# Kernel optimization log

Measured on AMD Instinct MI355X. Metric: run time of the kernel, lower is better.

The kernel has to match this reference:

```python
import jax, jax.numpy as jnp
import numpy as np

D_MODEL = 2048
NUM_HEADS = 16
D_K = D_MODEL // NUM_HEADS  # 128, per-head dim used for RoPE
ROPE_THETA = 10000.0
MAX_SEQ_LEN = 2048
BATCH = 4
SEQ = 2048


def _trunc_normal(key, shape, std):
    # approximate trunc_normal_(mean=0, std, a=-3std, b=3std)
    return jnp.clip(std * jax.random.normal(key, shape), -3 * std, 3 * std)


def setup_inputs() -> dict:
    key = jax.random.key(0)
    ks = jax.random.split(key, 6)
    x = jax.random.normal(ks[0], (BATCH, SEQ, D_MODEL), dtype=jnp.float32)
    token_positions = jnp.arange(SEQ, dtype=jnp.int32)
    std = float(np.sqrt(2.0 / (D_MODEL + D_MODEL)))
    wq = _trunc_normal(ks[1], (D_MODEL, D_MODEL), std)  # (d_out, d_in)
    wk = _trunc_normal(ks[2], (D_MODEL, D_MODEL), std)
    wv = _trunc_normal(ks[3], (D_MODEL, D_MODEL), std)
    wo = _trunc_normal(ks[4], (D_MODEL, D_MODEL), std)
    return {"x": x, "token_positions": token_positions,
            "wq": wq, "wk": wk, "wv": wv, "wo": wo}


def _rope(t, pos):
    # t: (b, h, n, d_k), pos: (n,) int
    # interleaved pairs: (x1, x2) = (t[..., 0::2], t[..., 1::2])
    freqs = 1.0 / (ROPE_THETA ** (jnp.arange(0, D_K, 2, dtype=jnp.float32) / D_K))
    angles = pos.astype(jnp.float32)[:, None] * freqs[None, :]  # (n, d_k/2)
    cos = jnp.cos(angles).astype(t.dtype)
    sin = jnp.sin(angles).astype(t.dtype)
    tr = t.reshape(*t.shape[:-1], D_K // 2, 2)
    x1, x2 = tr[..., 0], tr[..., 1]
    y1 = cos * x1 - sin * x2
    y2 = sin * x1 + cos * x2
    return jnp.stack([y1, y2], axis=-1).reshape(t.shape)


def reference(x, token_positions, wq, wk, wv, wo):
    b, n, d = x.shape
    q = jnp.einsum('bnd,od->bno', x, wq)
    k = jnp.einsum('bnd,od->bno', x, wk)
    v = jnp.einsum('bnd,od->bno', x, wv)
    # split heads for RoPE: (b, n, h*dk) -> (b, h, n, dk)
    split = lambda t: t.reshape(b, n, NUM_HEADS, D_K).transpose(0, 2, 1, 3)
    merge = lambda t: t.transpose(0, 2, 1, 3).reshape(b, n, d)
    q = merge(_rope(split(q), token_positions))
    k = merge(_rope(split(k), token_positions))
    # NOTE: source merges heads back BEFORE flash attention -> single-head
    # attention over full d_model with causal mask, scale 1/sqrt(d_model)
    scale = 1.0 / jnp.sqrt(jnp.asarray(d, dtype=x.dtype))
    scores = jnp.einsum('bqd,bkd->bqk', q, k) * scale  # (b, n, n)
    causal = jnp.tril(jnp.ones((n, n), dtype=bool))
    scores = jnp.where(causal[None, :, :], scores, jnp.finfo(scores.dtype).min)
    attn = jax.nn.softmax(scores, axis=-1)
    out = jnp.einsum('bqk,bkd->bqd', attn, v)
    return jnp.einsum('bnd,od->bno', out, wo)
```

## Files before the change

### kernel.cpp

```cpp
#include <hip/hip_runtime.h>
#include <hip/hip_bf16.h>
#include <cstdint>
#include <cmath>

typedef __attribute__((ext_vector_type(4))) float f32x4;
typedef __attribute__((ext_vector_type(8))) short bf16x8;

#define BAR()   __builtin_amdgcn_s_barrier()
#define PRIO1() __builtin_amdgcn_s_setprio(1)
#define PRIO0() __builtin_amdgcn_s_setprio(0)
#define WAITV6() asm volatile("s_waitcnt vmcnt(6)" ::: "memory")
#define WAITV4() asm volatile("s_waitcnt vmcnt(4)" ::: "memory")
#define WAITV0() asm volatile("s_waitcnt vmcnt(0)" ::: "memory")
#define MM(a,b,c) __builtin_amdgcn_mfma_f32_16x16x32_bf16((a),(b),(c),0,0,0)

__device__ __forceinline__ void gl_lds16(const __hip_bfloat16* g, char* l) {
    __builtin_amdgcn_global_load_lds(
        (const __attribute__((address_space(1))) void*)g,
        (__attribute__((address_space(3))) void*)l, 16, 0, 0);
}
__device__ __forceinline__ void store_c(float* C, size_t i, float v) { C[i] = v; }
__device__ __forceinline__ void store_c(__hip_bfloat16* C, size_t i, float v) { C[i] = __float2bfloat16(v); }

#define SGA8(dd, h, i, kt) do{ const int s_ = (h)*16 + (i)*8 + w; \
    gl_lds16(Asb + (size_t)((s_>>1)<<4) * lda + ((s_&1)<<5) + (kt), \
             lds + (dd)*65536 + (s_<<10)); }while(0)
#define SGB8N(dd, g, kt) do{ const int sB_ = (g)*8 + w; \
    const int hi_ = sB_ >> 4, r_ = sB_ & 15; \
    const int wc_ = r_ >> 2, ni_ = hi_*2 + ((r_>>1)&1), kk_ = r_ & 1; \
    gl_lds16(Bsb + (size_t)(wc_*64 + ni_*16) * ldb + (kk_<<5) + (kt), \
             lds + (dd)*65536 + 32768 + (sB_<<10)); }while(0)
#define LDA8(dd, miA, kk) (*(const bf16x8*)(lds + (dd)*65536 + ((sbA + (miA)*2 + (kk)) << 10) + rswz))
#define LDB8N(dd, ni, kk) (*(const bf16x8*)(lds + (dd)*65536 + 32768 + \
    ((((((ni)>>1)<<4) + ((w&3)<<2) + (((ni)&1)<<1) + (kk))) << 10) + rswz))

template<typename CT>
__global__ __launch_bounds__(512, 2)
void gemm8p(const __hip_bfloat16* __restrict__ A, const __hip_bfloat16* __restrict__ B,
            CT* __restrict__ C, int K, int lda, int ldb, int ldc, int nbx, float alpha)
{
    __shared__ __align__(1024) char lds[131072];

    const int nwg = gridDim.x;
    const int q8 = nwg >> 3, r8 = nwg & 7;
    const int xcd = blockIdx.x & 7, blk = blockIdx.x >> 3;
    const int wg = (xcd < r8 ? xcd * (q8 + 1) : r8 * (q8 + 1) + (xcd - r8) * q8) + blk;
    const int bm0 = (wg / nbx) * 256, bn0 = (wg % nbx) * 256;

    const int tid  = threadIdx.x;
    const int lane = tid & 63;
    const int w    = tid >> 6;

    const int rb   = (lane & 15) * 64 + (lane >> 4) * 16;
    const int rswz = rb ^ (((rb >> 9) & 1) << 5);
    const int sbA  = (w >> 2) * 16;

    const int l16 = lane * 16;
    const int uqs = l16 ^ (((l16 >> 9) & 1) << 5);
    const int rIn = uqs >> 6;
    const int cIn = (uqs & 63) >> 1;
    const __hip_bfloat16* Asb = A + (size_t)(bm0 + rIn) * lda + cIn;
    const __hip_bfloat16* Bsb = B + (size_t)(bn0 + rIn) * ldb + cIn;

    f32x4 acc[8][4] = {};
    bf16x8 afA[4][2], bfB[2][2];

    const int nt = K >> 6;

    SGA8(0, 0, 0, 0); SGA8(0, 1, 0, 0);
    SGB8N(0, 0, 0);   SGB8N(0, 1, 0);
    SGB8N(0, 2, 0);   SGB8N(0, 3, 0);
    SGA8(0, 0, 1, 0); SGA8(0, 1, 1, 0);
    if (nt > 1) {
        SGA8(1, 0, 0, 64); SGA8(1, 1, 0, 64);
        SGB8N(1, 2, 64);   SGB8N(1, 3, 64);
        SGA8(1, 0, 1, 64); SGA8(1, 1, 1, 64);
        WAITV6();
    } else WAITV0();
    BAR();

    for (int t = 0; t < nt; ++t) {
        const int d   = t & 1, e = d ^ 1;
        const bool p1 = (t + 1) < nt;
        const bool p2 = (t + 2) < nt;
        const int kt1 = (t + 1) << 6;
        const int kt2 = (t + 2) << 6;

#pragma unroll
        for (int mi = 0; mi < 4; ++mi) { afA[mi][0] = LDA8(d, mi, 0); afA[mi][1] = LDA8(d, mi, 1); }
#pragma unroll
        for (int ni = 0; ni < 2; ++ni) { bfB[ni][0] = LDB8N(d, ni, 0); bfB[ni][1] = LDB8N(d, ni, 1); }
        if (p1) { SGB8N(e, 0, kt1); SGB8N(e, 1, kt1); }
        BAR();
        PRIO1();
#pragma unroll
        for (int mi = 0; mi < 4; ++mi)
#pragma unroll
            for (int ni = 0; ni < 2; ++ni) {
                f32x4 c = acc[mi][ni];
                c = MM(afA[mi][0], bfB[ni][0], c);
                c = MM(afA[mi][1], bfB[ni][1], c);
                acc[mi][ni] = c;
            }
        PRIO0();
        BAR();

#pragma unroll
        for (int ni = 0; ni < 2; ++ni) { bfB[ni][0] = LDB8N(d, 2 + ni, 0); bfB[ni][1] = LDB8N(d, 2 + ni, 1); }
        if (p2) { SGA8(d, 0, 0, kt2); SGA8(d, 1, 0, kt2); }
        BAR();
        PRIO1();
#pragma unroll
        for (int mi = 0; mi < 4; ++mi)
#pragma unroll
            for (int ni = 0; ni < 2; ++ni) {
                f32x4 c = acc[mi][2 + ni];
                c = MM(afA[mi][0], bfB[ni][0], c);
                c = MM(afA[mi][1], bfB[ni][1], c);
                acc[mi][2 + ni] = c;
            }
        PRIO0();
        BAR();

#pragma unroll
        for (int mi = 0; mi < 4; ++mi) { afA[mi][0] = LDA8(d, 4 + mi, 0); afA[mi][1] = LDA8(d, 4 + mi, 1); }
        if (p2) { SGB8N(d, 2, kt2); SGB8N(d, 3, kt2); }
        BAR();
        PRIO1();
#pragma unroll
        for (int mi = 0; mi < 4; ++mi)
#pragma unroll
            for (int ni = 0; ni < 2; ++ni) {
                f32x4 c = acc[4 + mi][2 + ni];
                c = MM(afA[mi][0], bfB[ni][0], c);
                c = MM(afA[mi][1], bfB[ni][1], c);
                acc[4 + mi][2 + ni] = c;
            }
        PRIO0();
        BAR();

#pragma unroll
        for (int ni = 0; ni < 2; ++ni) { bfB[ni][0] = LDB8N(d, ni, 0); bfB[ni][1] = LDB8N(d, ni, 1); }
        if (p2) { SGA8(d, 0, 1, kt2); SGA8(d, 1, 1, kt2); WAITV6(); }
        else WAITV0();
        BAR();
        PRIO1();
#pragma unroll
        for (int mi = 0; mi < 4; ++mi)
#pragma unroll
            for (int ni = 0; ni < 2; ++ni) {
                f32x4 c = acc[4 + mi][ni];
                c = MM(afA[mi][0], bfB[ni][0], c);
                c = MM(afA[mi][1], bfB[ni][1], c);
                acc[4 + mi][ni] = c;
            }
        PRIO0();
        BAR();
    }

    const int cr = (lane >> 4) * 4, cc = lane & 15;
    const int wrow = bm0 + (w >> 2) * 128, wcol = bn0 + (w & 3) * 64;
#pragma unroll
    for (int mi = 0; mi < 8; ++mi)
#pragma unroll
        for (int ni = 0; ni < 4; ++ni) {
            const int row = wrow + mi * 16 + cr;
            const int col = wcol + ni * 16 + cc;
#pragma unroll
            for (int j = 0; j < 4; ++j)
                store_c(C, (size_t)(row + j) * ldc + col, acc[mi][ni][j] * alpha);
        }
}

#define STAGEA(nb, kt) do{ gl_lds16(Asrc + (kt),                        lds + (nb)         + wb); \
                           gl_lds16(Asrc + (size_t)128 * lda + (kt),    lds + (nb) +  8192 + wb);}while(0)
#define STAGEB(nb, kt) do{ gl_lds16(Bsrc + (kt),                        lds + (nb) + 16384 + wb); \
                           gl_lds16(Bsrc + (size_t)128 * ldb + (kt),    lds + (nb) + 24576 + wb);}while(0)

template<typename CT, int MODE>
__global__ __launch_bounds__(512, 2)
void gemm256(const __hip_bfloat16* __restrict__ A, const __hip_bfloat16* __restrict__ B,
             CT* __restrict__ C, int K, int lda, int ldb, int ldc, int nbx,
             float alpha, size_t sA, size_t sB, size_t sC)
{
    __shared__ __align__(1024) char lds[98304];

    int bm0, bn0;
    if (MODE == 1) {
        const int wgi = blockIdx.x;
        int by = (int)((sqrtf(8.f * wgi + 1.f) - 1.f) * 0.5f);
        if (by * (by + 1) / 2 > wgi) --by;
        if ((by + 1) * (by + 2) / 2 <= wgi) ++by;
        const int bx = wgi - by * (by + 1) / 2;
        bm0 = by * 256; bn0 = bx * 256;
    } else if (MODE == 2) {
        const int g = blockIdx.x;
        const int nby = gridDim.x / nbx;
        const int bx = g % nbx;
        const int by = (g / nbx + bx) % nby;
        bm0 = by * 256; bn0 = bx * 256;
    } else {
        const int nwg = gridDim.x;
        const int q8 = nwg >> 3, r8 = nwg & 7;
        const int xcd = blockIdx.x & 7, blk = blockIdx.x >> 3;
        const int wg = (xcd < r8 ? xcd * (q8 + 1) : r8 * (q8 + 1) + (xcd - r8) * q8) + blk;
        bm0 = (wg / nbx) * 256; bn0 = (wg % nbx) * 256;
    }

    A += sA * blockIdx.y; B += sB * blockIdx.y; C += sC * blockIdx.y;

    const int tid  = threadIdx.x;
    const int lane = tid & 63;
    const int w    = tid >> 6;
    const int wb   = w * 1024;

    const int rb   = (lane & 15) * 64 + (lane >> 4) * 16;
    const int rswz = rb ^ (((rb >> 9) & 1) << 5);
    const int srA  = (w >> 2) * 8;
    const int srB  = (w & 3) * 4;

    const int q0 = tid * 16;
    const int uq = q0 ^ (((q0 >> 9) & 1) << 5);
    const int r0 = ((q0 >> 10) << 4) | ((uq >> 6) & 15);
    const int c0 = (uq & 63) >> 1;
    const __hip_bfloat16* Asrc = A + (size_t)(bm0 + r0) * lda + c0;
    const __hip_bfloat16* Bsrc = B + (size_t)(bn0 + r0) * ldb + c0;

    f32x4 acc[8][4] = {};
    bf16x8 af[4], bf[4];

    const int klim = bm0 + 256;
    const int kend = (MODE == 2) ? (K < klim ? K : klim) : K;
    const int nt   = kend >> 5;

    STAGEA(0, 0); STAGEB(0, 0);
    if (nt > 1) { STAGEA(32768, 32); STAGEB(32768, 32); }

    for (int t = 0; t < nt; ++t) {
        if (t + 1 < nt) WAITV4(); else WAITV0();
        BAR();
        const char* dA = lds + (t % 3) * 32768;
        const char* dB = dA + 16384;
        const int  nbo = ((t + 2) % 3) * 32768;
        const bool pf  = (t + 2 < nt);
        const int  kt  = (t + 2) << 5;

#pragma unroll
        for (int i = 0; i < 4; ++i) af[i] = *(const bf16x8*)(dA + ((srA + i) << 10) + rswz);
#pragma unroll
        for (int i = 0; i < 4; ++i) bf[i] = *(const bf16x8*)(dB + ((srB + i) << 10) + rswz);
        if (pf) STAGEA(nbo, kt);
        BAR();
        PRIO1();
#pragma unroll
        for (int mi = 0; mi < 4; ++mi)
#pragma unroll
            for (int ni = 0; ni < 4; ++ni)
                acc[mi][ni] = MM(af[mi], bf[ni], acc[mi][ni]);
        PRIO0();

#pragma unroll
        for (int i = 0; i < 4; ++i) af[i] = *(const bf16x8*)(dA + ((srA + 4 + i) << 10) + rswz);
        if (pf) STAGEB(nbo, kt);
        BAR();
        PRIO1();
#pragma unroll
        for (int mi = 0; mi < 4; ++mi)
#pragma unroll
            for (int ni = 0; ni < 4; ++ni)
                acc[4 + mi][ni] = MM(af[mi], bf[ni], acc[4 + mi][ni]);
        PRIO0();
    }

    const int cr = (lane >> 4) * 4, cc = lane & 15;
    const int wrow = bm0 + (w >> 2) * 128, wcol = bn0 + (w & 3) * 64;
#pragma unroll
    for (int mi = 0; mi < 8; ++mi)
#pragma unroll
        for (int ni = 0; ni < 4; ++ni) {
            const int row = wrow + mi * 16 + cr;
            const int col = wcol + ni * 16 + cc;
#pragma unroll
            for (int j = 0; j < 4; ++j)
                store_c(C, (size_t)(row + j) * ldc + col, acc[mi][ni][j] * alpha);
        }
}

__global__ void f32_to_bf16_vec(const float* __restrict__ in,
                                __hip_bfloat16* __restrict__ out, int n4)
{
    int i = blockIdx.x * 256 + threadIdx.x;
    if (i >= n4) return;
    float4 v = ((const float4*)in)[i];
    union { ushort4 u; __hip_bfloat16 h[4]; } o;
    o.h[0] = __float2bfloat16(v.x);
    o.h[1] = __float2bfloat16(v.y);
    o.h[2] = __float2bfloat16(v.z);
    o.h[3] = __float2bfloat16(v.w);
    ((ushort4*)out)[i] = o.u;
}

__global__ void conv_w4(const float* __restrict__ w0, const float* __restrict__ w1,
                        const float* __restrict__ w2, const float* __restrict__ w3,
                        __hip_bfloat16* o0, __hip_bfloat16* o1,
                        __hip_bfloat16* o2, __hip_bfloat16* o3, int n4)
{
    int i = blockIdx.x * 256 + threadIdx.x;
    if (i >= n4) return;
    const float* src; __hip_bfloat16* dst;
    switch (blockIdx.y) {
        case 0: src = w0; dst = o0; break;
        case 1: src = w1; dst = o1; break;
        case 2: src = w2; dst = o2; break;
        default: src = w3; dst = o3; break;
    }
    float4 v = ((const float4*)src)[i];
    union { ushort4 u; __hip_bfloat16 h[4]; } o;
    o.h[0] = __float2bfloat16(v.x);
    o.h[1] = __float2bfloat16(v.y);
    o.h[2] = __float2bfloat16(v.z);
    o.h[3] = __float2bfloat16(v.w);
    ((ushort4*)dst)[i] = o.u;
}

__global__ void rope_table(const int* __restrict__ pos, float2* __restrict__ tab, int N)
{
    int i = blockIdx.x * 256 + threadIdx.x;
    if (i >= N * 64) return;
    int n = i >> 6, j = i & 63;
    float p = (float)pos[n];
    float ang = p * powf(10000.f, -(float)j * (1.0f / 64.0f));
    tab[i] = make_float2(cosf(ang), sinf(ang));
}

__global__ void rope_apply2(__hip_bfloat16* __restrict__ Q, __hip_bfloat16* __restrict__ K,
                            const float2* __restrict__ tab, int ld)
{
    int i = blockIdx.x * 256 + threadIdx.x;
    __hip_bfloat16* T = blockIdx.y ? K : Q;
    int r  = i >> 8;
    int cb = (i & 255) << 3;
    int n  = r & 2047;
    int j0 = (cb >> 1) & 63;
    union { bf16x8 v; __hip_bfloat162 h[4]; } u;
    __hip_bfloat16* p = T + (size_t)r * ld + cb;
    u.v = *(const bf16x8*)p;
#pragma unroll
    for (int k = 0; k < 4; ++k) {
        float2 cs = tab[(n << 6) + j0 + k];
        float x1 = __bfloat162float(u.h[k].x);
        float x2 = __bfloat162float(u.h[k].y);
        u.h[k].x = __float2bfloat16(cs.x * x1 - cs.y * x2);
        u.h[k].y = __float2bfloat16(cs.y * x1 + cs.x * x2);
    }
    *(bf16x8*)p = u.v;
}

__global__ void softmax_causal_ip(float* __restrict__ S, int N)
{
    const int q = blockIdx.x;
    float* srow = S + ((size_t)blockIdx.y * N + q) * N;
    __shared__ float buf[2048];
    __shared__ float red[8];
    const int tid = threadIdx.x;
    const int wend = ((q >> 8) + 1) << 8;

    float4* b4 = (float4*)buf;
    const float4* s4 = (const float4*)srow;
    for (int i = tid; i <= (q >> 2); i += 256) b4[i] = s4[i];
    __syncthreads();

    float m = -1e30f;
    for (int j = tid; j <= q; j += 256) m = fmaxf(m, buf[j]);
#pragma unroll
    for (int o = 32; o > 0; o >>= 1) m = fmaxf(m, __shfl_xor(m, o));
    if ((tid & 63) == 0) red[tid >> 6] = m;
    __syncthreads();
    m = fmaxf(fmaxf(red[0], red[1]), fmaxf(red[2], red[3]));

    float sum = 0.f;
    for (int j = tid; j <= q; j += 256) { float e = __expf(buf[j] - m); buf[j] = e; sum += e; }
#pragma unroll
    for (int o = 32; o > 0; o >>= 1) sum += __shfl_xor(sum, o);
    if ((tid & 63) == 0) red[4 + (tid >> 6)] = sum;
    __syncthreads();
    const float inv = 1.f / (red[4] + red[5] + red[6] + red[7]);

    __hip_bfloat162* p2 = (__hip_bfloat162*)srow;
    for (int i = tid; i < (wend >> 1); i += 256) {
        int j0 = i * 2;
        __hip_bfloat162 h;
        h.x = __float2bfloat16(j0     <= q ? buf[j0]     * inv : 0.f);
        h.y = __float2bfloat16(j0 + 1 <= q ? buf[j0 + 1] * inv : 0.f);
        p2[i] = h;
    }
}

__global__ void transpose_bf16(const __hip_bfloat16* __restrict__ V,
                               __hip_bfloat16* __restrict__ Vt, int N, int ldv)
{
    __shared__ __hip_bfloat16 tile[32][33];
    const size_t bi = (size_t)blockIdx.z * N * ldv;
    const size_t bo = (size_t)blockIdx.z * N * N;
    const int k0 = blockIdx.x * 32, d0 = blockIdx.y * 32;
    const int tx = threadIdx.x, ty = threadIdx.y;
#pragma unroll
    for (int j = 0; j < 4; ++j)
        tile[ty + 8 * j][tx] = V[bi + (size_t)(k0 + ty + 8 * j) * ldv + d0 + tx];
    __syncthreads();
#pragma unroll
    for (int j = 0; j < 4; ++j)
        Vt[bo + (size_t)(d0 + ty + 8 * j) * N + k0 + tx] = tile[tx][ty + 8 * j];
}

extern "C" void kernel_launch(void* const* d_in, const int* in_sizes, int n_in,
                              void* d_out, int out_size, void* d_ws, size_t ws_size,
                              hipStream_t stream)
{
    const float* x  = (const float*)d_in[0];
    const int* pos  = (const int*)d_in[1];
    const float* wq = (const float*)d_in[2];
    const float* wk = (const float*)d_in[3];
    const float* wv = (const float*)d_in[4];
    const float* wo = (const float*)d_in[5];
    float* out = (float*)d_out;

    const int B = 4, N = 2048, D = 2048;
    const int M = B * N;
    const int D3 = 3 * D;
    const size_t MB = 1ull << 20;
    if (ws_size < 192 * MB) return;

    char* w = (char*)d_ws;
    __hip_bfloat16* QKV  = (__hip_bfloat16*)(w + 0 * MB);
    __hip_bfloat16* wqkv = (__hip_bfloat16*)(w + 96 * MB);
    __hip_bfloat16* wob  = (__hip_bfloat16*)(w + 120 * MB);
    __hip_bfloat16* xb   = (__hip_bfloat16*)(w + 128 * MB);
    __hip_bfloat16* Vt   = xb;
    __hip_bfloat16* AO   = (__hip_bfloat16*)(w + 160 * MB);
    float2*         tab  = (float2*)(w + 190 * MB);

    __hip_bfloat16* Qb = QKV;
    __hip_bfloat16* Kb = QKV + D;
    __hip_bfloat16* Vb = QKV + 2 * D;

    float* Sal = (float*)d_out;

    f32_to_bf16_vec<<<(M * D / 4 + 255) / 256, 256, 0, stream>>>(x, xb, M * D / 4);
    conv_w4<<<dim3((D * D / 4 + 255) / 256, 4), 256, 0, stream>>>(
        wq, wk, wv, wo, wqkv, wqkv + (size_t)D * D, wqkv + (size_t)2 * D * D, wob, D * D / 4);
    rope_table<<<(N * 64 + 255) / 256, 256, 0, stream>>>(pos, tab, N);

    gemm8p<__hip_bfloat16><<<dim3((D3 / 256) * (M / 256)), 512, 0, stream>>>(
        xb, wqkv, QKV, D, D, D, D3, D3 / 256, 1.f);

    rope_apply2<<<dim3(M, 2), 256, 0, stream>>>(Qb, Kb, tab, D3);

    transpose_bf16<<<dim3(N / 32, N / 32, B), dim3(32, 8), 0, stream>>>(Vb, Vt, N, D3);

    const float scale = 1.0f / sqrtf((float)D);
    const int nbxA = N / 256;
    const int ntri = nbxA * (nbxA + 1) / 2;
    gemm256<float, 1><<<dim3(ntri, B), 512, 0, stream>>>(
        Qb, Kb, Sal, D, D3, D3, N, nbxA, scale,
        (size_t)N * D3, (size_t)N * D3, (size_t)N * N);
    softmax_causal_ip<<<dim3(N, B), 256, 0, stream>>>(Sal, N);
    gemm256<__hip_bfloat16, 2><<<dim3(nbxA * nbxA, B), 512, 0, stream>>>(
        (const __hip_bfloat16*)Sal, Vt, AO, N, 2 * N, N, D, nbxA, 1.f,
        (size_t)2 * N * N, (size_t)N * N, (size_t)N * D);

    gemm256<float, 0><<<dim3((D / 256) * (M / 256)), 512, 0, stream>>>(
        AO, wob, out, D, D, D, D, D / 256, 1.f, 0, 0, 0);
}
```

Before: 463.1 us.

## Unify GEMMs into one 64-wide-K kernel with register-prefetched LDS fragments

Merges the two GEMM kernels into a single templated gemm8p that carries gemm256's MODE-based block mapping (triangular, causal-limited K, plain). The K tile grows from 32 to 64. The loop uses double-buffered register fragments (afA0/afA1, bfB0/bfB1) so the LDS reads for the next phase are issued during the current MFMA block instead of before it, which is meant to hide LDS latency behind matrix math. This raises LDS use to 128KB and increases register pressure, and the QK^T, PV and output-projection GEMMs now all go through this schedule.

```diff
diff --git a/kernel.cpp b/kernel.cpp
--- a/kernel.cpp
+++ b/kernel.cpp
@@ -9,8 +9,8 @@
 #define BAR()   __builtin_amdgcn_s_barrier()
 #define PRIO1() __builtin_amdgcn_s_setprio(1)
 #define PRIO0() __builtin_amdgcn_s_setprio(0)
+#define WAITV8() asm volatile("s_waitcnt vmcnt(8)" ::: "memory")
 #define WAITV6() asm volatile("s_waitcnt vmcnt(6)" ::: "memory")
-#define WAITV4() asm volatile("s_waitcnt vmcnt(4)" ::: "memory")
 #define WAITV0() asm volatile("s_waitcnt vmcnt(0)" ::: "memory")
 #define MM(a,b,c) __builtin_amdgcn_mfma_f32_16x16x32_bf16((a),(b),(c),0,0,0)
 
@@ -34,156 +34,13 @@
 #define LDB8N(dd, ni, kk) (*(const bf16x8*)(lds + (dd)*65536 + 32768 + \
     ((((((ni)>>1)<<4) + ((w&3)<<2) + (((ni)&1)<<1) + (kk))) << 10) + rswz))
 
-template<typename CT>
+template<typename CT, int MODE>
 __global__ __launch_bounds__(512, 2)
 void gemm8p(const __hip_bfloat16* __restrict__ A, const __hip_bfloat16* __restrict__ B,
-            CT* __restrict__ C, int K, int lda, int ldb, int ldc, int nbx, float alpha)
+            CT* __restrict__ C, int K, int lda, int ldb, int ldc, int nbx,
+            float alpha, size_t sA, size_t sB, size_t sC)
 {
     __shared__ __align__(1024) char lds[131072];
-
-    const int nwg = gridDim.x;
-    const int q8 = nwg >> 3, r8 = nwg & 7;
-    const int xcd = blockIdx.x & 7, blk = blockIdx.x >> 3;
-    const int wg = (xcd < r8 ? xcd * (q8 + 1) : r8 * (q8 + 1) + (xcd - r8) * q8) + blk;
-    const int bm0 = (wg / nbx) * 256, bn0 = (wg % nbx) * 256;
-
-    const int tid  = threadIdx.x;
-    const int lane = tid & 63;
-    const int w    = tid >> 6;
-
-    const int rb   = (lane & 15) * 64 + (lane >> 4) * 16;
-    const int rswz = rb ^ (((rb >> 9) & 1) << 5);
-    const int sbA  = (w >> 2) * 16;
-
-    const int l16 = lane * 16;
-    const int uqs = l16 ^ (((l16 >> 9) & 1) << 5);
-    const int rIn = uqs >> 6;
-    const int cIn = (uqs & 63) >> 1;
-    const __hip_bfloat16* Asb = A + (size_t)(bm0 + rIn) * lda + cIn;
-    const __hip_bfloat16* Bsb = B + (size_t)(bn0 + rIn) * ldb + cIn;
-
-    f32x4 acc[8][4] = {};
-    bf16x8 afA[4][2], bfB[2][2];
-
-    const int nt = K >> 6;
-
-    SGA8(0, 0, 0, 0); SGA8(0, 1, 0, 0);
-    SGB8N(0, 0, 0);   SGB8N(0, 1, 0);
-    SGB8N(0, 2, 0);   SGB8N(0, 3, 0);
-    SGA8(0, 0, 1, 0); SGA8(0, 1, 1, 0);
-    if (nt > 1) {
-        SGA8(1, 0, 0, 64); SGA8(1, 1, 0, 64);
-        SGB8N(1, 2, 64);   SGB8N(1, 3, 64);
-        SGA8(1, 0, 1, 64); SGA8(1, 1, 1, 64);
-        WAITV6();
-    } else WAITV0();
-    BAR();
-
-    for (int t = 0; t < nt; ++t) {
-        const int d   = t & 1, e = d ^ 1;
-        const bool p1 = (t + 1) < nt;
-        const bool p2 = (t + 2) < nt;
-        const int kt1 = (t + 1) << 6;
-        const int kt2 = (t + 2) << 6;
-
-#pragma unroll
-        for (int mi = 0; mi < 4; ++mi) { afA[mi][0] = LDA8(d, mi, 0); afA[mi][1] = LDA8(d, mi, 1); }
-#pragma unroll
-        for (int ni = 0; ni < 2; ++ni) { bfB[ni][0] = LDB8N(d, ni, 0); bfB[ni][1] = LDB8N(d, ni, 1); }
-        if (p1) { SGB8N(e, 0, kt1); SGB8N(e, 1, kt1); }
-        BAR();
-        PRIO1();
-#pragma unroll
-        for (int mi = 0; mi < 4; ++mi)
-#pragma unroll
-            for (int ni = 0; ni < 2; ++ni) {
-                f32x4 c = acc[mi][ni];
-                c = MM(afA[mi][0], bfB[ni][0], c);
-                c = MM(afA[mi][1], bfB[ni][1], c);
-                acc[mi][ni] = c;
-            }
-        PRIO0();
-        BAR();
-
-#pragma unroll
-        for (int ni = 0; ni < 2; ++ni) { bfB[ni][0] = LDB8N(d, 2 + ni, 0); bfB[ni][1] = LDB8N(d, 2 + ni, 1); }
-        if (p2) { SGA8(d, 0, 0, kt2); SGA8(d, 1, 0, kt2); }
-        BAR();
-        PRIO1();
-#pragma unroll
-        for (int mi = 0; mi < 4; ++mi)
-#pragma unroll
-            for (int ni = 0; ni < 2; ++ni) {
-                f32x4 c = acc[mi][2 + ni];
-                c = MM(afA[mi][0], bfB[ni][0], c);
-                c = MM(afA[mi][1], bfB[ni][1], c);
-                acc[mi][2 + ni] = c;
-            }
-        PRIO0();
-        BAR();
-
-#pragma unroll
-        for (int mi = 0; mi < 4; ++mi) { afA[mi][0] = LDA8(d, 4 + mi, 0); afA[mi][1] = LDA8(d, 4 + mi, 1); }
-        if (p2) { SGB8N(d, 2, kt2); SGB8N(d, 3, kt2); }
-        BAR();
-        PRIO1();
-#pragma unroll
-        for (int mi = 0; mi < 4; ++mi)
-#pragma unroll
-            for (int ni = 0; ni < 2; ++ni) {
-                f32x4 c = acc[4 + mi][2 + ni];
-                c = MM(afA[mi][0], bfB[ni][0], c);
-                c = MM(afA[mi][1], bfB[ni][1], c);
-                acc[4 + mi][2 + ni] = c;
-            }
-        PRIO0();
-        BAR();
-
-#pragma unroll
-        for (int ni = 0; ni < 2; ++ni) { bfB[ni][0] = LDB8N(d, ni, 0); bfB[ni][1] = LDB8N(d, ni, 1); }
-        if (p2) { SGA8(d, 0, 1, kt2); SGA8(d, 1, 1, kt2); WAITV6(); }
-        else WAITV0();
-        BAR();
-        PRIO1();
-#pragma unroll
-        for (int mi = 0; mi < 4; ++mi)
-#pragma unroll
-            for (int ni = 0; ni < 2; ++ni) {
-                f32x4 c = acc[4 + mi][ni];
-                c = MM(afA[mi][0], bfB[ni][0], c);
-                c = MM(afA[mi][1], bfB[ni][1], c);
-                acc[4 + mi][ni] = c;
-            }
-        PRIO0();
-        BAR();
-    }
-
-    const int cr = (lane >> 4) * 4, cc = lane & 15;
-    const int wrow = bm0 + (w >> 2) * 128, wcol = bn0 + (w & 3) * 64;
-#pragma unroll
-    for (int mi = 0; mi < 8; ++mi)
-#pragma unroll
-        for (int ni = 0; ni < 4; ++ni) {
-            const int row = wrow + mi * 16 + cr;
-            const int col = wcol + ni * 16 + cc;
-#pragma unroll
-            for (int j = 0; j < 4; ++j)
-                store_c(C, (size_t)(row + j) * ldc + col, acc[mi][ni][j] * alpha);
-        }
-}
-
-#define STAGEA(nb, kt) do{ gl_lds16(Asrc + (kt),                        lds + (nb)         + wb); \
-                           gl_lds16(Asrc + (size_t)128 * lda + (kt),    lds + (nb) +  8192 + wb);}while(0)
-#define STAGEB(nb, kt) do{ gl_lds16(Bsrc + (kt),                        lds + (nb) + 16384 + wb); \
-                           gl_lds16(Bsrc + (size_t)128 * ldb + (kt),    lds + (nb) + 24576 + wb);}while(0)
-
-template<typename CT, int MODE>
-__global__ __launch_bounds__(512, 2)
-void gemm256(const __hip_bfloat16* __restrict__ A, const __hip_bfloat16* __restrict__ B,
-             CT* __restrict__ C, int K, int lda, int ldb, int ldc, int nbx,
-             float alpha, size_t sA, size_t sB, size_t sC)
-{
-    __shared__ __align__(1024) char lds[98304];
 
     int bm0, bn0;
     if (MODE == 1) {
@@ -212,64 +69,122 @@
     const int tid  = threadIdx.x;
     const int lane = tid & 63;
     const int w    = tid >> 6;
-    const int wb   = w * 1024;
 
     const int rb   = (lane & 15) * 64 + (lane >> 4) * 16;
     const int rswz = rb ^ (((rb >> 9) & 1) << 5);
-    const int srA  = (w >> 2) * 8;
-    const int srB  = (w & 3) * 4;
-
-    const int q0 = tid * 16;
-    const int uq = q0 ^ (((q0 >> 9) & 1) << 5);
-    const int r0 = ((q0 >> 10) << 4) | ((uq >> 6) & 15);
-    const int c0 = (uq & 63) >> 1;
-    const __hip_bfloat16* Asrc = A + (size_t)(bm0 + r0) * lda + c0;
-    const __hip_bfloat16* Bsrc = B + (size_t)(bn0 + r0) * ldb + c0;
+    const int sbA  = (w >> 2) * 16;
+
+    const int l16 = lane * 16;
+    const int uqs = l16 ^ (((l16 >> 9) & 1) << 5);
+    const int rIn = uqs >> 6;
+    const int cIn = (uqs & 63) >> 1;
+    const __hip_bfloat16* Asb = A + (size_t)(bm0 + rIn) * lda + cIn;
+    const __hip_bfloat16* Bsb = B + (size_t)(bn0 + rIn) * ldb + cIn;
 
     f32x4 acc[8][4] = {};
-    bf16x8 af[4], bf[4];
+    bf16x8 afA0[4][2], afA1[4][2], bfB0[2][2], bfB1[2][2];
 
     const int klim = bm0 + 256;
     const int kend = (MODE == 2) ? (K < klim ? K : klim) : K;
-    const int nt   = kend >> 5;
-
-    STAGEA(0, 0); STAGEB(0, 0);
-    if (nt > 1) { STAGEA(32768, 32); STAGEB(32768, 32); }
+    const int nt   = kend >> 6;
+
+    SGA8(0, 0, 0, 0); SGA8(0, 1, 0, 0);
+    SGB8N(0, 0, 0);   SGB8N(0, 1, 0);
+    SGB8N(0, 2, 0);   SGB8N(0, 3, 0);
+    SGA8(0, 0, 1, 0); SGA8(0, 1, 1, 0);
+    if (nt > 1) {
+        SGA8(1, 0, 0, 64); SGA8(1, 1, 0, 64);
+        SGB8N(1, 2, 64);   SGB8N(1, 3, 64);
+        SGA8(1, 0, 1, 64); SGA8(1, 1, 1, 64);
+        WAITV6();
+    } else WAITV0();
+    BAR();
+#pragma unroll
+    for (int mi = 0; mi < 4; ++mi) { afA0[mi][0] = LDA8(0, mi, 0); afA0[mi][1] = LDA8(0, mi, 1); }
+#pragma unroll
+    for (int ni = 0; ni < 2; ++ni) { bfB0[ni][0] = LDB8N(0, ni, 0); bfB0[ni][1] = LDB8N(0, ni, 1); }
 
     for (int t = 0; t < nt; ++t) {
-        if (t + 1 < nt) WAITV4(); else WAITV0();
-        BAR();
-        const char* dA = lds + (t % 3) * 32768;
-        const char* dB = dA + 16384;
-        const int  nbo = ((t + 2) % 3) * 32768;
-        const bool pf  = (t + 2 < nt);
-        const int  kt  = (t + 2) << 5;
-
-#pragma unroll
-        for (int i = 0; i < 4; ++i) af[i] = *(const bf16x8*)(dA + ((srA + i) << 10) + rswz);
-#pragma unroll
-        for (int i = 0; i < 4; ++i) bf[i] = *(const bf16x8*)(dB + ((srB + i) << 10) + rswz);
-        if (pf) STAGEA(nbo, kt);
+        const int d   = t & 1, e = d ^ 1;
+        const bool p1 = (t + 1) < nt;
+        const bool p2 = (t + 2) < nt;
+        const int kt1 = (t + 1) << 6;
+        const int kt2 = (t + 2) << 6;
+
+        if (p1) { SGB8N(e, 0, kt1); SGB8N(e, 1, kt1); }
         BAR();
         PRIO1();
 #pragma unroll
         for (int mi = 0; mi < 4; ++mi)
 #pragma unroll
-            for (int ni = 0; ni < 4; ++ni)
-                acc[mi][ni] = MM(af[mi], bf[ni], acc[mi][ni]);
+            for (int ni = 0; ni < 2; ++ni) {
+                f32x4 c = acc[mi][ni];
+                c = MM(afA0[mi][0], bfB0[ni][0], c);
+                c = MM(afA0[mi][1], bfB0[ni][1], c);
+                acc[mi][ni] = c;
+            }
+#pragma unroll
+        for (int ni = 0; ni < 2; ++ni) { bfB1[ni][0] = LDB8N(d, 2 + ni, 0); bfB1[ni][1] = LDB8N(d, 2 + ni, 1); }
         PRIO0();
-
-#pragma unroll
-        for (int i = 0; i < 4; ++i) af[i] = *(const bf16x8*)(dA + ((srA + 4 + i) << 10) + rswz);
-        if (pf) STAGEB(nbo, kt);
+        BAR();
+
+        if (p2) { SGA8(d, 0, 0, kt2); SGA8(d, 1, 0, kt2); WAITV8(); }
+        else if (p1) WAITV6();
+        else WAITV0();
         BAR();
         PRIO1();
 #pragma unroll
         for (int mi = 0; mi < 4; ++mi)
 #pragma unroll
-            for (int ni = 0; ni < 4; ++ni)
-                acc[4 + mi][ni] = MM(af[mi], bf[ni], acc[4 + mi][ni]);
+            for (int ni = 0; ni < 2; ++ni) {
+                f32x4 c = acc[mi][2 + ni];
+                c = MM(afA0[mi][0], bfB1[ni][0], c);
+                c = MM(afA0[mi][1], bfB1[ni][1], c);
+                acc[mi][2 + ni] = c;
+            }
+#pragma unroll
+        for (int mi = 0; mi < 4; ++mi) { afA1[mi][0] = LDA8(d, 4 + mi, 0); afA1[mi][1] = LDA8(d, 4 + mi, 1); }
         PRIO0();
+        BAR();
+
+        if (p2) { SGB8N(d, 2, kt2); SGB8N(d, 3, kt2); }
+        BAR();
+        PRIO1();
+#pragma unroll
+        for (int mi = 0; mi < 4; ++mi)
+#pragma unroll
+            for (int ni = 0; ni < 2; ++ni) {
+                f32x4 c = acc[4 + mi][2 + ni];
+                c = MM(afA1[mi][0], bfB1[ni][0], c);
+                c = MM(afA1[mi][1], bfB1[ni][1], c);
+                acc[4 + mi][2 + ni] = c;
+            }
+        if (p1) {
+#pragma unroll
+            for (int mi = 0; mi < 4; ++mi) { afA0[mi][0] = LDA8(e, mi, 0); afA0[mi][1] = LDA8(e, mi, 1); }
+        }
+        PRIO0();
+        BAR();
+
+        if (p2) { SGA8(d, 0, 1, kt2); SGA8(d, 1, 1, kt2); WAITV6(); }
+        else WAITV0();
+        BAR();
+        PRIO1();
+#pragma unroll
+        for (int mi = 0; mi < 4; ++mi)
+#pragma unroll
+            for (int ni = 0; ni < 2; ++ni) {
+                f32x4 c = acc[4 + mi][ni];
+                c = MM(afA1[mi][0], bfB0[ni][0], c);
+                c = MM(afA1[mi][1], bfB0[ni][1], c);
+                acc[4 + mi][ni] = c;
+            }
+        if (p1) {
+#pragma unroll
+            for (int ni = 0; ni < 2; ++ni) { bfB0[ni][0] = LDB8N(e, ni, 0); bfB0[ni][1] = LDB8N(e, ni, 1); }
+        }
+        PRIO0();
+        BAR();
     }
 
     const int cr = (lane >> 4) * 4, cc = lane & 15;
@@ -451,8 +366,8 @@
         wq, wk, wv, wo, wqkv, wqkv + (size_t)D * D, wqkv + (size_t)2 * D * D, wob, D * D / 4);
     rope_table<<<(N * 64 + 255) / 256, 256, 0, stream>>>(pos, tab, N);
 
-    gemm8p<__hip_bfloat16><<<dim3((D3 / 256) * (M / 256)), 512, 0, stream>>>(
-        xb, wqkv, QKV, D, D, D, D3, D3 / 256, 1.f);
+    gemm8p<__hip_bfloat16, 0><<<dim3((D3 / 256) * (M / 256)), 512, 0, stream>>>(
+        xb, wqkv, QKV, D, D, D, D3, D3 / 256, 1.f, 0, 0, 0);
 
     rope_apply2<<<dim3(M, 2), 256, 0, stream>>>(Qb, Kb, tab, D3);
 
@@ -461,14 +376,14 @@
     const float scale = 1.0f / sqrtf((float)D);
     const int nbxA = N / 256;
     const int ntri = nbxA * (nbxA + 1) / 2;
-    gemm256<float, 1><<<dim3(ntri, B), 512, 0, stream>>>(
+    gemm8p<float, 1><<<dim3(ntri, B), 512, 0, stream>>>(
         Qb, Kb, Sal, D, D3, D3, N, nbxA, scale,
         (size_t)N * D3, (size_t)N * D3, (size_t)N * N);
     softmax_causal_ip<<<dim3(N, B), 256, 0, stream>>>(Sal, N);
-    gemm256<__hip_bfloat16, 2><<<dim3(nbxA * nbxA, B), 512, 0, stream>>>(
+    gemm8p<__hip_bfloat16, 2><<<dim3(nbxA * nbxA, B), 512, 0, stream>>>(
         (const __hip_bfloat16*)Sal, Vt, AO, N, 2 * N, N, D, nbxA, 1.f,
         (size_t)2 * N * N, (size_t)N * N, (size_t)N * D);
 
-    gemm256<float, 0><<<dim3((D / 256) * (M / 256)), 512, 0, stream>>>(
+    gemm8p<float, 0><<<dim3((D / 256) * (M / 256)), 512, 0, stream>>>(
         AO, wob, out, D, D, D, D, D / 256, 1.f, 0, 0, 0);
 }
```

New measurement: 461.8 us. About the same (-0.3%).
